# Optimization experiments

Measured on AMD Instinct MI355X. Metric: run time of the kernel, lower is better.

## Reference

```python
import jax, jax.numpy as jnp
import numpy as np

GRID_SIZE = 32
GRID_BOUND = 0.5


def point_closest_cell_index(points):
    grid_min = -GRID_BOUND + GRID_BOUND / GRID_SIZE
    inds = (points - grid_min) * GRID_SIZE / (2.0 * GRID_BOUND)
    return jnp.round(jnp.clip(inds, 0.0, GRID_SIZE - 1))


def cal_distance(trans_points, cp, voxel, weight=1.0):
    # trans_points: [B,N,3], cp: [B,G^3,3], voxel: [B,G^3] (0/1 occupancy)
    nb = point_closest_cell_index(trans_points)  # [B,N,3]
    strides = jnp.array([GRID_SIZE ** 2, GRID_SIZE, 1], dtype=trans_points.dtype)
    idx = (nb @ strides).astype(jnp.int32)  # [B,N] flattened voxel index
    mask = 1.0 - jnp.take_along_axis(voxel, idx, axis=1)  # [B,N]
    closest = jnp.take_along_axis(cp, idx[..., None], axis=1)  # [B,N,3]
    d = (trans_points - closest) * mask[..., None]
    return jnp.mean(jnp.sum(d * d, axis=(1, 2))) * weight


def plane_sym_transform(points, p):
    # reflect points across plane n.x + d = 0; p = [nx,ny,nz,d]
    n, d = p[:3], p[3]
    dist = (points @ n + d) / jnp.sum(n * n)
    return points - 2.0 * dist[..., None] * n


def rot_sym_transform(points, q):
    # rotate points by (normalized) quaternion q = [w,x,y,z]
    q = q / jnp.sqrt(jnp.sum(q * q))
    w, u = q[0], q[1:]
    t = 2.0 * jnp.cross(jnp.broadcast_to(u, points.shape), points)
    return points + w * t + jnp.cross(jnp.broadcast_to(u, t.shape), t)


def setup_inputs() -> dict:
    key = jax.random.key(0)
    ks = jax.random.split(key, 5)
    B, N, G3 = 256, 4096, GRID_SIZE ** 3
    points = jax.random.normal(ks[0], (B, N, 3), jnp.float32) * 0.25
    cp = jax.random.normal(ks[1], (B, G3, 3), jnp.float32) * 0.25
    voxel = (jax.random.uniform(ks[2], (B, G3), jnp.float32) < 0.2).astype(jnp.float32)
    plane = jax.random.normal(ks[3], (3, 4), jnp.float32)
    quat = jax.random.normal(ks[4], (3, 4), jnp.float32)
    return {"points": points, "cp": cp, "voxel": voxel, "plane": plane, "quat": quat}


def reference(points, cp, voxel, plane, quat):
    ref_loss = jnp.zeros((1,), points.dtype)
    rot_loss = jnp.zeros((1,), points.dtype)
    for i in range(plane.shape[0]):
        ref_points = plane_sym_transform(points, plane[i])
        ref_loss = ref_loss + cal_distance(ref_points, cp, voxel)
    for i in range(quat.shape[0]):
        rot_points = rot_sym_transform(points, quat[i])
        rot_loss = rot_loss + cal_distance(rot_points, cp, voxel)
    return ref_loss, rot_loss
```

## Files before the change

kernel.cpp:

```cpp
#include <hip/hip_runtime.h>
#include <hip/hip_fp16.h>

#define G3 32768
#define SLABS 2
#define SLAB_CELLS 16384
#define TPB 1024

typedef float f32x4 __attribute__((ext_vector_type(4)));

static __device__ __forceinline__ unsigned pack2h(float a, float b) {
    unsigned short ua = __half_as_ushort(__float2half(a));
    unsigned short ub = __half_as_ushort(__float2half(b));
    return (unsigned)ua | ((unsigned)ub << 16);
}
static __device__ __forceinline__ float lo2f(unsigned u) {
    return __half2float(__ushort_as_half((unsigned short)(u & 0xffffu)));
}
static __device__ __forceinline__ float hi2f(unsigned u) {
    return __half2float(__ushort_as_half((unsigned short)(u >> 16)));
}

#define PROCESS(PX, PY, PZ, ACCR_EXPR, ACCQ_EXPR)                                   \
    do {                                                                            \
        _Pragma("unroll")                                                           \
        for (int t = 0; t < 3; ++t) {                                               \
                                        \
            float dist = ((PX)*pnx[t] + (PY)*pny[t] + (PZ)*pnz[t] + pdd[t]) * pinv[t]; \
            float rx = (PX) - 2.0f * dist * pnx[t];                                 \
            float ry = (PY) - 2.0f * dist * pny[t];                                 \
            float rz = (PZ) - 2.0f * dist * pnz[t];                                 \
            {                                                                       \
                float fx = rintf(fminf(fmaxf((rx - gmin) * 32.0f, 0.0f), 31.0f));   \
                float fy = rintf(fminf(fmaxf((ry - gmin) * 32.0f, 0.0f), 31.0f));   \
                float fz = rintf(fminf(fmaxf((rz - gmin) * 32.0f, 0.0f), 31.0f));   \
                int local = (int)(fx * 1024.0f + fy * 32.0f + fz) - base;           \
                if ((unsigned)local < SLAB_CELLS) {                                 \
                    uint2 u = slab[local];                                          \
                    float m  = hi2f(u.y);                                           \
                    float dx = (rx - lo2f(u.x)) * m;                                \
                    float dy = (ry - hi2f(u.x)) * m;                                \
                    float dz = (rz - lo2f(u.y)) * m;                                \
                    ACCR_EXPR += dx*dx + dy*dy + dz*dz;                             \
                }                                                                   \
            }                                                                       \
                                     \
            float tx = 2.0f * (quy[t]*(PZ) - quz[t]*(PY));                          \
            float ty = 2.0f * (quz[t]*(PX) - qux[t]*(PZ));                          \
            float tz = 2.0f * (qux[t]*(PY) - quy[t]*(PX));                          \
            float ox = (PX) + qw[t]*tx + (quy[t]*tz - quz[t]*ty);                   \
            float oy = (PY) + qw[t]*ty + (quz[t]*tx - qux[t]*tz);                   \
            float oz = (PZ) + qw[t]*tz + (qux[t]*ty - quy[t]*tx);                   \
            {                                                                       \
                float fx = rintf(fminf(fmaxf((ox - gmin) * 32.0f, 0.0f), 31.0f));   \
                float fy = rintf(fminf(fmaxf((oy - gmin) * 32.0f, 0.0f), 31.0f));   \
                float fz = rintf(fminf(fmaxf((oz - gmin) * 32.0f, 0.0f), 31.0f));   \
                int local = (int)(fx * 1024.0f + fy * 32.0f + fz) - base;           \
                if ((unsigned)local < SLAB_CELLS) {                                 \
                    uint2 u = slab[local];                                          \
                    float m  = hi2f(u.y);                                           \
                    float dx = (ox - lo2f(u.x)) * m;                                \
                    float dy = (oy - hi2f(u.x)) * m;                                \
                    float dz = (oz - lo2f(u.y)) * m;                                \
                    ACCQ_EXPR += dx*dx + dy*dy + dz*dz;                             \
                }                                                                   \
            }                                                                       \
        }                                                                           \
    } while (0)

__global__ __launch_bounds__(TPB)
void symloss_slab_kernel(const float* __restrict__ points,
                         const float* __restrict__ cp,
                         const float* __restrict__ voxel,
                         const float* __restrict__ plane,
                         const float* __restrict__ quat,
                         float* __restrict__ out,
                         int N, float invB)
{
    __shared__ uint2 slab[SLAB_CELLS];
    __shared__ float sR[TPB / 64], sQ[TPB / 64];

    const int row  = blockIdx.x >> 1;
    const int base = (blockIdx.x & 1) * SLAB_CELLS;

    const float* __restrict__ cpb  = cp     + (size_t)row * (G3 * 3) + (size_t)base * 3;
    const float* __restrict__ voxb = voxel  + (size_t)row * G3 + base;
    const float* __restrict__ ptb  = points + (size_t)row * (size_t)N * 3;

    const float4* __restrict__ pt4 = reinterpret_cast<const float4*>(ptb);
    const int ngrp = N >> 2;
    float4 q0, q1, q2;
    const bool havePts = (int)threadIdx.x < ngrp;
    if (havePts) {
        q0 = pt4[3 * threadIdx.x + 0];
        q1 = pt4[3 * threadIdx.x + 1];
        q2 = pt4[3 * threadIdx.x + 2];
    }

    float pnx[3], pny[3], pnz[3], pdd[3], pinv[3];
    float qw[3], qux[3], quy[3], quz[3];
#pragma unroll
    for (int i = 0; i < 3; ++i) {
        float nx = plane[4*i+0], ny = plane[4*i+1], nz = plane[4*i+2], dd = plane[4*i+3];
        pnx[i] = nx; pny[i] = ny; pnz[i] = nz; pdd[i] = dd;
        pinv[i] = 1.0f / (nx*nx + ny*ny + nz*nz);

        float w  = quat[4*i+0], ux = quat[4*i+1], uy = quat[4*i+2], uz = quat[4*i+3];
        float rn = 1.0f / sqrtf(w*w + ux*ux + uy*uy + uz*uz);
        qw[i] = w*rn; qux[i] = ux*rn; quy[i] = uy*rn; quz[i] = uz*rn;
    }

    const f32x4* __restrict__ cp4 = reinterpret_cast<const f32x4*>(cpb);
    const f32x4* __restrict__ vx4 = reinterpret_cast<const f32x4*>(voxb);
#pragma unroll 2
    for (int gI = threadIdx.x; gI < SLAB_CELLS / 4; gI += TPB) {
        f32x4 v0 = __builtin_nontemporal_load(&cp4[3*gI+0]);
        f32x4 v1 = __builtin_nontemporal_load(&cp4[3*gI+1]);
        f32x4 v2 = __builtin_nontemporal_load(&cp4[3*gI+2]);
        f32x4 w  = __builtin_nontemporal_load(&vx4[gI]);
        uint2 c0; c0.x = pack2h(v0.x, v0.y); c0.y = pack2h(v0.z, 1.0f - w.x);
        uint2 c1; c1.x = pack2h(v0.w, v1.x); c1.y = pack2h(v1.y, 1.0f - w.y);
        uint2 c2; c2.x = pack2h(v1.z, v1.w); c2.y = pack2h(v2.x, 1.0f - w.z);
        uint2 c3; c3.x = pack2h(v2.y, v2.z); c3.y = pack2h(v2.w, 1.0f - w.w);
        slab[4*gI+0] = c0; slab[4*gI+1] = c1;
        slab[4*gI+2] = c2; slab[4*gI+3] = c3;
    }
    __syncthreads();

    const float gmin = -0.484375f;
    float accR = 0.0f, accQ = 0.0f;

    if (havePts) {
        PROCESS(q0.x, q0.y, q0.z, accR, accQ);
        PROCESS(q0.w, q1.x, q1.y, accR, accQ);
        PROCESS(q1.z, q1.w, q2.x, accR, accQ);
        PROCESS(q2.y, q2.z, q2.w, accR, accQ);
    }
    for (int g4 = threadIdx.x + TPB; g4 < ngrp; g4 += TPB) {
        float4 a0 = pt4[3*g4+0], a1 = pt4[3*g4+1], a2 = pt4[3*g4+2];
        PROCESS(a0.x, a0.y, a0.z, accR, accQ);
        PROCESS(a0.w, a1.x, a1.y, accR, accQ);
        PROCESS(a1.z, a1.w, a2.x, accR, accQ);
        PROCESS(a2.y, a2.z, a2.w, accR, accQ);
    }

#pragma unroll
    for (int off = 32; off > 0; off >>= 1) {
        accR += __shfl_down(accR, off, 64);
        accQ += __shfl_down(accQ, off, 64);
    }
    int wave = threadIdx.x >> 6;
    int lane = threadIdx.x & 63;
    if (lane == 0) { sR[wave] = accR; sQ[wave] = accQ; }
    __syncthreads();
    if (threadIdx.x == 0) {
        float r = 0.0f, q = 0.0f;
#pragma unroll
        for (int w = 0; w < TPB / 64; ++w) { r += sR[w]; q += sQ[w]; }
        atomicAdd(&out[0], r * invB);
        atomicAdd(&out[1], q * invB);
    }
}

extern "C" void kernel_launch(void* const* d_in, const int* in_sizes, int n_in,
                              void* d_out, int out_size, void* d_ws, size_t ws_size,
                              hipStream_t stream)
{
    const float* points = (const float*)d_in[0];
    const float* cp     = (const float*)d_in[1];
    const float* voxel  = (const float*)d_in[2];
    const float* plane  = (const float*)d_in[3];
    const float* quat   = (const float*)d_in[4];
    float* out = (float*)d_out;

    int B = in_sizes[2] / G3;
    int N = (in_sizes[0] / 3) / B;
    float invB = 1.0f / (float)B;

    (void)hipMemsetAsync(out, 0, (size_t)out_size * sizeof(float), stream);

    symloss_slab_kernel<<<B * SLABS, TPB, 0, stream>>>(points, cp, voxel, plane, quat,
                                                       out, N, invB);
}
```

Measured before the change: 207.1 us.

## Process both voxel slabs in one block per row with branchless gathers

Each block now handles a whole batch row and loops over the two 16K-cell slabs, reloading shared memory between passes, instead of launching two blocks per row. Points are read once per row rather than once per slab-block, and the out-of-slab branch becomes a predicated gather that reads cell 0 and applies a zero mask. In exchange the grid has half as many blocks. Each block also runs two serial phases separated by barriers, so the slab load and the compute for one row no longer overlap across blocks. Transform math is still computed twice per point.

After: 243.2 us. 1.17x slower.

```diff
diff --git a/kernel.cpp b/kernel.cpp
--- a/kernel.cpp
+++ b/kernel.cpp
@@ -2,7 +2,6 @@
 #include <hip/hip_fp16.h>
 
 #define G3 32768
-#define SLABS 2
 #define SLAB_CELLS 16384
 #define TPB 1024
 
@@ -20,70 +19,56 @@
     return __half2float(__ushort_as_half((unsigned short)(u >> 16)));
 }
 
-#define PROCESS(PX, PY, PZ, ACCR_EXPR, ACCQ_EXPR)                                   \
-    do {                                                                            \
-        _Pragma("unroll")                                                           \
-        for (int t = 0; t < 3; ++t) {                                               \
-                                        \
+#define GATHER(RX, RY, RZ, ACC)                                                 \
+    {                                                                           \
+        float fx = rintf(fminf(fmaxf(((RX) - gmin) * 32.0f, 0.0f), 31.0f));     \
+        float fy = rintf(fminf(fmaxf(((RY) - gmin) * 32.0f, 0.0f), 31.0f));     \
+        float fz = rintf(fminf(fmaxf(((RZ) - gmin) * 32.0f, 0.0f), 31.0f));     \
+        int local = (int)(fx * 1024.0f + fy * 32.0f + fz) - base;               \
+        bool inb = (unsigned)local < (unsigned)SLAB_CELLS;                      \
+        uint2 u = slab[inb ? local : 0];                                        \
+        float m  = inb ? hi2f(u.y) : 0.0f;                                      \
+        float dx = ((RX) - lo2f(u.x)) * m;                                      \
+        float dy = ((RY) - hi2f(u.x)) * m;                                      \
+        float dz = ((RZ) - lo2f(u.y)) * m;                                      \
+        ACC += dx*dx + dy*dy + dz*dz;                                           \
+    }
+
+#define PROCESS(PX, PY, PZ)                                                     \
+    do {                                                                        \
+        _Pragma("unroll")                                                       \
+        for (int t = 0; t < 3; ++t) {                                           \
             float dist = ((PX)*pnx[t] + (PY)*pny[t] + (PZ)*pnz[t] + pdd[t]) * pinv[t]; \
-            float rx = (PX) - 2.0f * dist * pnx[t];                                 \
-            float ry = (PY) - 2.0f * dist * pny[t];                                 \
-            float rz = (PZ) - 2.0f * dist * pnz[t];                                 \
-            {                                                                       \
-                float fx = rintf(fminf(fmaxf((rx - gmin) * 32.0f, 0.0f), 31.0f));   \
-                float fy = rintf(fminf(fmaxf((ry - gmin) * 32.0f, 0.0f), 31.0f));   \
-                float fz = rintf(fminf(fmaxf((rz - gmin) * 32.0f, 0.0f), 31.0f));   \
-                int local = (int)(fx * 1024.0f + fy * 32.0f + fz) - base;           \
-                if ((unsigned)local < SLAB_CELLS) {                                 \
-                    uint2 u = slab[local];                                          \
-                    float m  = hi2f(u.y);                                           \
-                    float dx = (rx - lo2f(u.x)) * m;                                \
-                    float dy = (ry - hi2f(u.x)) * m;                                \
-                    float dz = (rz - lo2f(u.y)) * m;                                \
-                    ACCR_EXPR += dx*dx + dy*dy + dz*dz;                             \
-                }                                                                   \
-            }                                                                       \
-                                     \
-            float tx = 2.0f * (quy[t]*(PZ) - quz[t]*(PY));                          \
-            float ty = 2.0f * (quz[t]*(PX) - qux[t]*(PZ));                          \
-            float tz = 2.0f * (qux[t]*(PY) - quy[t]*(PX));                          \
-            float ox = (PX) + qw[t]*tx + (quy[t]*tz - quz[t]*ty);                   \
-            float oy = (PY) + qw[t]*ty + (quz[t]*tx - qux[t]*tz);                   \
-            float oz = (PZ) + qw[t]*tz + (qux[t]*ty - quy[t]*tx);                   \
-            {                                                                       \
-                float fx = rintf(fminf(fmaxf((ox - gmin) * 32.0f, 0.0f), 31.0f));   \
-                float fy = rintf(fminf(fmaxf((oy - gmin) * 32.0f, 0.0f), 31.0f));   \
-                float fz = rintf(fminf(fmaxf((oz - gmin) * 32.0f, 0.0f), 31.0f));   \
-                int local = (int)(fx * 1024.0f + fy * 32.0f + fz) - base;           \
-                if ((unsigned)local < SLAB_CELLS) {                                 \
-                    uint2 u = slab[local];                                          \
-                    float m  = hi2f(u.y);                                           \
-                    float dx = (ox - lo2f(u.x)) * m;                                \
-                    float dy = (oy - hi2f(u.x)) * m;                                \
-                    float dz = (oz - lo2f(u.y)) * m;                                \
-                    ACCQ_EXPR += dx*dx + dy*dy + dz*dz;                             \
-                }                                                                   \
-            }                                                                       \
-        }                                                                           \
+            float rx = (PX) - 2.0f * dist * pnx[t];                             \
+            float ry = (PY) - 2.0f * dist * pny[t];                             \
+            float rz = (PZ) - 2.0f * dist * pnz[t];                             \
+            GATHER(rx, ry, rz, accR);                                           \
+            float tx = 2.0f * (quy[t]*(PZ) - quz[t]*(PY));                      \
+            float ty = 2.0f * (quz[t]*(PX) - qux[t]*(PZ));                      \
+            float tz = 2.0f * (qux[t]*(PY) - quy[t]*(PX));                      \
+            float ox = (PX) + qw[t]*tx + (quy[t]*tz - quz[t]*ty);               \
+            float oy = (PY) + qw[t]*ty + (quz[t]*tx - qux[t]*tz);               \
+            float oz = (PZ) + qw[t]*tz + (qux[t]*ty - quy[t]*tx);               \
+            GATHER(ox, oy, oz, accQ);                                           \
+        }                                                                       \
     } while (0)
 
 __global__ __launch_bounds__(TPB)
-void symloss_slab_kernel(const float* __restrict__ points,
-                         const float* __restrict__ cp,
-                         const float* __restrict__ voxel,
-                         const float* __restrict__ plane,
-                         const float* __restrict__ quat,
-                         float* __restrict__ out,
-                         int N, float invB)
+void symloss_row_kernel(const float* __restrict__ points,
+                        const float* __restrict__ cp,
+                        const float* __restrict__ voxel,
+                        const float* __restrict__ plane,
+                        const float* __restrict__ quat,
+                        float* __restrict__ out,
+                        int N, float invB)
 {
     __shared__ uint2 slab[SLAB_CELLS];
     __shared__ float sR[TPB / 64], sQ[TPB / 64];
 
-    const int row  = blockIdx.x >> 1;
-    const int base = (blockIdx.x & 1) * SLAB_CELLS;
+    const int row = blockIdx.x;
 
-    const float* __restrict__ cpb  = cp     + (size_t)row * (G3 * 3) + (size_t)base * 3;
-    const float* __restrict__ voxb = voxel  + (size_t)row * G3 + base;
+    const float* __restrict__ cpb  = cp     + (size_t)row * (G3 * 3);
+    const float* __restrict__ voxb = voxel  + (size_t)row * G3;
     const float* __restrict__ ptb  = points + (size_t)row * (size_t)N * 3;
 
     const float4* __restrict__ pt4 = reinterpret_cast<const float4*>(ptb);
@@ -109,38 +94,43 @@
         qw[i] = w*rn; qux[i] = ux*rn; quy[i] = uy*rn; quz[i] = uz*rn;
     }
 
-    const f32x4* __restrict__ cp4 = reinterpret_cast<const f32x4*>(cpb);
-    const f32x4* __restrict__ vx4 = reinterpret_cast<const f32x4*>(voxb);
-#pragma unroll 2
-    for (int gI = threadIdx.x; gI < SLAB_CELLS / 4; gI += TPB) {
-        f32x4 v0 = __builtin_nontemporal_load(&cp4[3*gI+0]);
-        f32x4 v1 = __builtin_nontemporal_load(&cp4[3*gI+1]);
-        f32x4 v2 = __builtin_nontemporal_load(&cp4[3*gI+2]);
-        f32x4 w  = __builtin_nontemporal_load(&vx4[gI]);
-        uint2 c0; c0.x = pack2h(v0.x, v0.y); c0.y = pack2h(v0.z, 1.0f - w.x);
-        uint2 c1; c1.x = pack2h(v0.w, v1.x); c1.y = pack2h(v1.y, 1.0f - w.y);
-        uint2 c2; c2.x = pack2h(v1.z, v1.w); c2.y = pack2h(v2.x, 1.0f - w.z);
-        uint2 c3; c3.x = pack2h(v2.y, v2.z); c3.y = pack2h(v2.w, 1.0f - w.w);
-        slab[4*gI+0] = c0; slab[4*gI+1] = c1;
-        slab[4*gI+2] = c2; slab[4*gI+3] = c3;
-    }
-    __syncthreads();
-
     const float gmin = -0.484375f;
     float accR = 0.0f, accQ = 0.0f;
 
-    if (havePts) {
-        PROCESS(q0.x, q0.y, q0.z, accR, accQ);
-        PROCESS(q0.w, q1.x, q1.y, accR, accQ);
-        PROCESS(q1.z, q1.w, q2.x, accR, accQ);
-        PROCESS(q2.y, q2.z, q2.w, accR, accQ);
-    }
-    for (int g4 = threadIdx.x + TPB; g4 < ngrp; g4 += TPB) {
-        float4 a0 = pt4[3*g4+0], a1 = pt4[3*g4+1], a2 = pt4[3*g4+2];
-        PROCESS(a0.x, a0.y, a0.z, accR, accQ);
-        PROCESS(a0.w, a1.x, a1.y, accR, accQ);
-        PROCESS(a1.z, a1.w, a2.x, accR, accQ);
-        PROCESS(a2.y, a2.z, a2.w, accR, accQ);
+    for (int s = 0; s < 2; ++s) {
+        const int base = s * SLAB_CELLS;
+
+        const f32x4* __restrict__ cp4 = reinterpret_cast<const f32x4*>(cpb + (size_t)base * 3);
+        const f32x4* __restrict__ vx4 = reinterpret_cast<const f32x4*>(voxb + base);
+#pragma unroll 2
+        for (int gI = threadIdx.x; gI < SLAB_CELLS / 4; gI += TPB) {
+            f32x4 v0 = __builtin_nontemporal_load(&cp4[3*gI+0]);
+            f32x4 v1 = __builtin_nontemporal_load(&cp4[3*gI+1]);
+            f32x4 v2 = __builtin_nontemporal_load(&cp4[3*gI+2]);
+            f32x4 w  = __builtin_nontemporal_load(&vx4[gI]);
+            uint2 c0; c0.x = pack2h(v0.x, v0.y); c0.y = pack2h(v0.z, 1.0f - w.x);
+            uint2 c1; c1.x = pack2h(v0.w, v1.x); c1.y = pack2h(v1.y, 1.0f - w.y);
+            uint2 c2; c2.x = pack2h(v1.z, v1.w); c2.y = pack2h(v2.x, 1.0f - w.z);
+            uint2 c3; c3.x = pack2h(v2.y, v2.z); c3.y = pack2h(v2.w, 1.0f - w.w);
+            slab[4*gI+0] = c0; slab[4*gI+1] = c1;
+            slab[4*gI+2] = c2; slab[4*gI+3] = c3;
+        }
+        __syncthreads();
+
+        if (havePts) {
+            PROCESS(q0.x, q0.y, q0.z);
+            PROCESS(q0.w, q1.x, q1.y);
+            PROCESS(q1.z, q1.w, q2.x);
+            PROCESS(q2.y, q2.z, q2.w);
+        }
+        for (int g4 = threadIdx.x + TPB; g4 < ngrp; g4 += TPB) {
+            float4 a0 = pt4[3*g4+0], a1 = pt4[3*g4+1], a2 = pt4[3*g4+2];
+            PROCESS(a0.x, a0.y, a0.z);
+            PROCESS(a0.w, a1.x, a1.y);
+            PROCESS(a1.z, a1.w, a2.x);
+            PROCESS(a2.y, a2.z, a2.w);
+        }
+        __syncthreads();
     }
 
 #pragma unroll
@@ -178,6 +168,6 @@
 
     (void)hipMemsetAsync(out, 0, (size_t)out_size * sizeof(float), stream);
 
-    symloss_slab_kernel<<<B * SLABS, TPB, 0, stream>>>(points, cp, voxel, plane, quat,
-                                                       out, N, invB);
+    symloss_row_kernel<<<B, TPB, 0, stream>>>(points, cp, voxel, plane, quat,
+                                              out, N, invB);
 }
```
